# Performance work log

Hardware: AMD Instinct MI355X
Metric: run time of the kernel (lower is better)

The kernel has to match this reference:

```python
import jax, jax.numpy as jnp
import numpy as np

N_NODES = 50000
N_EDGES = 800000
D_IN = 1024
D_OUT = 256
LEAKY_SLOPE = 0.01  # F.leaky_relu default


def setup_inputs() -> dict:
    key = jax.random.key(0)
    k_x, k_w, k_b, k_src, k_dst, k_ew, k_norm = jax.random.split(key, 7)
    x = jax.random.normal(k_x, (N_NODES, D_IN), dtype=jnp.float32)
    # xavier_uniform-style scale for the weight
    limit = np.sqrt(6.0 / (D_IN + D_OUT)).astype(np.float32)
    weight = jax.random.uniform(k_w, (D_IN, D_OUT), dtype=jnp.float32, minval=-limit, maxval=limit)
    stdv = 1.0 / np.sqrt(D_OUT)
    bias = jax.random.uniform(k_b, (D_OUT,), dtype=jnp.float32, minval=-stdv, maxval=stdv)
    src = jax.random.randint(k_src, (N_EDGES,), 0, N_NODES, dtype=jnp.int64)
    dst = jax.random.randint(k_dst, (N_EDGES,), 0, N_NODES, dtype=jnp.int64)
    edge_index = jnp.stack([src, dst], axis=0)  # [2, E]
    edge_weight = jax.random.uniform(k_ew, (N_EDGES,), dtype=jnp.float32)
    norm = jax.random.uniform(k_norm, (N_NODES, 1), dtype=jnp.float32) + 0.5  # avoid div-by-~0
    return {"x": x, "weight": weight, "bias": bias, "edge_index": edge_index,
            "edge_weight": edge_weight, "norm": norm}


def reference(x, weight, bias, edge_index, edge_weight, norm):
    # support = input @ W            [N, D_OUT]
    support = x @ weight
    src = edge_index[0]
    dst = edge_index[1]
    # spmm(adj, support): out[i] = sum_{e: dst_e == i} w_e * support[src_e]
    msgs = support[src] * edge_weight[:, None]            # [E, D_OUT]
    out = jax.ops.segment_sum(msgs, dst, num_segments=x.shape[0])  # [N, D_OUT]
    out = out / norm + bias
    return jax.nn.leaky_relu(out, negative_slope=LEAKY_SLOPE)
```

## Files before the change

kernel.cpp:

```cpp
#include <hip/hip_runtime.h>
#include <hip/hip_bf16.h>

#define N_NODES 50000
#define N_EDGES 800000
#define D_IN    1024
#define D_OUT   256
#define CAP     64
#define LEAKY   0.01f

typedef __attribute__((ext_vector_type(8))) short bf16x8;
typedef __attribute__((ext_vector_type(4))) float f32x4;
typedef __attribute__((ext_vector_type(4))) int   i32x4;
typedef unsigned short u16;

__device__ __forceinline__ u16 f2bfu(float f) {
  uint32_t x = __float_as_uint(f);
  uint32_t r = (x + 0x7FFFu + ((x >> 16) & 1u)) >> 16;
  return (u16)r;
}
__device__ __forceinline__ float bfu2f(u16 u) {
  return __uint_as_float(((uint32_t)u) << 16);
}
__device__ __forceinline__ int swz(int b) { return b ^ (((b >> 7) & 7) << 4); }

__device__ __forceinline__ void gll16(const void* g, void* l) {
  __builtin_amdgcn_global_load_lds(
      (const __attribute__((address_space(1))) uint32_t*)g,
      (__attribute__((address_space(3))) uint32_t*)l, 16, 0, 0);
}

__global__ __launch_bounds__(256) void wconv_kernel(const float* __restrict__ w,
                                                    char* __restrict__ img,
                                                    int* __restrict__ deg) {
  const int t   = blockIdx.x * 256 + threadIdx.x;
  if (t < N_NODES) deg[t] = 0;
  const int t2 = t + 32768;
  if (t2 < N_NODES) deg[t2] = 0;

  const int n   = t & 255;
  const int kc  = (t >> 8) * 8;
  const int kt  = kc >> 6;
  const int kin = kc & 63;
  bf16x8 v;
#pragma unroll
  for (int i = 0; i < 8; ++i) v[i] = (short)f2bfu(w[(size_t)(kc + i) * D_OUT + n]);
  *(bf16x8*)(img + kt * 32768 + swz(n * 128 + kin * 2)) = v;
}

#define BM 64
#define BK 64
#define KSTEPS (D_IN / BK)
#define GEMM_BLOCKS ((N_NODES + BM - 1) / BM)
#define BUILD_BLOCKS 64

__global__ __launch_bounds__(512) void gemm_build_kernel(
    const float* __restrict__ x, const char* __restrict__ img,
    u16* __restrict__ support,
    const int* __restrict__ ei, const float* __restrict__ ew,
    int* __restrict__ deg, int2* __restrict__ csr) {
  __shared__ u16 Wbuf[2][16384];
  __shared__ u16 Xbuf[2][4096];

  if (blockIdx.x < BUILD_BLOCKS) {
    const int t0 = blockIdx.x * 512 + threadIdx.x;
    for (int e = t0; e < N_EDGES; e += BUILD_BLOCKS * 512) {
      const int src = ei[e];
      const int dst = ei[N_EDGES + e];
      const float w = ew[e];
      const int slot = atomicAdd(&deg[dst], 1);
      if (slot < CAP) {
        csr[dst * CAP + slot] = make_int2(src, __float_as_int(w));
      }
    }
    return;
  }

  const int tid  = threadIdx.x;
  const int lane = tid & 63;
  const int wid  = tid >> 6;
  const int wn   = wid & 3;
  const int wm   = wid >> 2;
  const int l15  = lane & 15;
  const int l16  = lane >> 4;
  const int m0   = (blockIdx.x - BUILD_BLOCKS) * BM;

  f32x4 acc[4][2];
#pragma unroll
  for (int i = 0; i < 4; ++i)
#pragma unroll
    for (int j = 0; j < 2; ++j) acc[i][j] = (f32x4)0.0f;

  const int xrow = tid >> 3;
  const int xk8  = (tid & 7) * 8;
  const int xrg  = min(m0 + xrow, N_NODES - 1);
  const float* xp = x + (size_t)xrg * D_IN + xk8;
  const int xw_off = swz(xrow * 128 + xk8 * 2);

  int a_off[2][4], b_off[2][2];
#pragma unroll
  for (int ks = 0; ks < 2; ++ks) {
#pragma unroll
    for (int i = 0; i < 4; ++i)
      a_off[ks][i] = swz((wn * 64 + i * 16 + l15) * 128 + ks * 64 + l16 * 16);
#pragma unroll
    for (int j = 0; j < 2; ++j)
      b_off[ks][j] = swz((wm * 32 + j * 16 + l15) * 128 + ks * 64 + l16 * 16);
  }

#pragma unroll
  for (int r = 0; r < 4; ++r)
    gll16(img + r * 8192 + tid * 16, (char*)&Wbuf[0][0] + r * 8192 + tid * 16);
  {
    const float4 xa = *(const float4*)(xp);
    const float4 xb = *(const float4*)(xp + 4);
    bf16x8 xv;
    xv[0] = (short)f2bfu(xa.x); xv[1] = (short)f2bfu(xa.y);
    xv[2] = (short)f2bfu(xa.z); xv[3] = (short)f2bfu(xa.w);
    xv[4] = (short)f2bfu(xb.x); xv[5] = (short)f2bfu(xb.y);
    xv[6] = (short)f2bfu(xb.z); xv[7] = (short)f2bfu(xb.w);
    *(bf16x8*)((char*)&Xbuf[0][0] + xw_off) = xv;
  }
  __syncthreads();

  for (int kt = 0; kt < KSTEPS; ++kt) {
    const int cur = kt & 1;
    float4 xa, xb;
    if (kt < KSTEPS - 1) {
#pragma unroll
      for (int r = 0; r < 4; ++r)
        gll16(img + (size_t)(kt + 1) * 32768 + r * 8192 + tid * 16,
              (char*)&Wbuf[cur ^ 1][0] + r * 8192 + tid * 16);
      xa = *(const float4*)(xp + (kt + 1) * BK);
      xb = *(const float4*)(xp + (kt + 1) * BK + 4);
    }

#pragma unroll
    for (int ks = 0; ks < 2; ++ks) {
      bf16x8 af[4], bfr[2];
#pragma unroll
      for (int i = 0; i < 4; ++i)
        af[i] = *(const bf16x8*)((const char*)&Wbuf[cur][0] + a_off[ks][i]);
#pragma unroll
      for (int j = 0; j < 2; ++j)
        bfr[j] = *(const bf16x8*)((const char*)&Xbuf[cur][0] + b_off[ks][j]);
#pragma unroll
      for (int i = 0; i < 4; ++i)
#pragma unroll
        for (int j = 0; j < 2; ++j)
          acc[i][j] = __builtin_amdgcn_mfma_f32_16x16x32_bf16(af[i], bfr[j], acc[i][j], 0, 0, 0);
    }

    if (kt < KSTEPS - 1) {
      bf16x8 xv;
      xv[0] = (short)f2bfu(xa.x); xv[1] = (short)f2bfu(xa.y);
      xv[2] = (short)f2bfu(xa.z); xv[3] = (short)f2bfu(xa.w);
      xv[4] = (short)f2bfu(xb.x); xv[5] = (short)f2bfu(xb.y);
      xv[6] = (short)f2bfu(xb.z); xv[7] = (short)f2bfu(xb.w);
      *(bf16x8*)((char*)&Xbuf[cur ^ 1][0] + xw_off) = xv;
    }
    __syncthreads();
  }

#pragma unroll
  for (int j = 0; j < 2; ++j) {
    const int m = m0 + wm * 32 + j * 16 + l15;
    if (m < N_NODES) {
#pragma unroll
      for (int i = 0; i < 4; ++i) {
        const int n = wn * 64 + i * 16 + l16 * 4;
        ushort4 o;
        o.x = f2bfu(acc[i][j][0]);
        o.y = f2bfu(acc[i][j][1]);
        o.z = f2bfu(acc[i][j][2]);
        o.w = f2bfu(acc[i][j][3]);
        *(ushort4*)&support[(size_t)m * D_OUT + n] = o;
      }
    }
  }
}

__global__ __launch_bounds__(256) void agg_kernel(const u16* __restrict__ support,
                                                  const int* __restrict__ deg,
                                                  const int2* __restrict__ csr,
                                                  const float* __restrict__ norm,
                                                  const float* __restrict__ bias,
                                                  float* __restrict__ out) {
  const int lane = threadIdx.x & 63;
  const int wid  = threadIdx.x >> 6;
  const int node = blockIdx.x * 4 + wid;
  const int d    = min(deg[node], CAP);
  const int cb   = node * CAP;
  const int ch   = lane * 4;

  float a0 = 0.f, a1 = 0.f, a2 = 0.f, a3 = 0.f;
  int s = 0;

  for (; s + 16 <= d; s += 16) {
    i32x4 q[8];
#pragma unroll
    for (int i = 0; i < 8; ++i)
      q[i] = __builtin_nontemporal_load((const i32x4*)&csr[cb + s + 2 * i]);
    ushort4 v[16];
#pragma unroll
    for (int i = 0; i < 8; ++i) {
      v[2 * i]     = *(const ushort4*)&support[(size_t)q[i][0] * D_OUT + ch];
      v[2 * i + 1] = *(const ushort4*)&support[(size_t)q[i][2] * D_OUT + ch];
    }
#pragma unroll
    for (int i = 0; i < 8; ++i) {
      const float wa = __int_as_float(q[i][1]);
      const float wb = __int_as_float(q[i][3]);
      a0 = fmaf(wa, bfu2f(v[2 * i].x), a0);
      a1 = fmaf(wa, bfu2f(v[2 * i].y), a1);
      a2 = fmaf(wa, bfu2f(v[2 * i].z), a2);
      a3 = fmaf(wa, bfu2f(v[2 * i].w), a3);
      a0 = fmaf(wb, bfu2f(v[2 * i + 1].x), a0);
      a1 = fmaf(wb, bfu2f(v[2 * i + 1].y), a1);
      a2 = fmaf(wb, bfu2f(v[2 * i + 1].z), a2);
      a3 = fmaf(wb, bfu2f(v[2 * i + 1].w), a3);
    }
  }

  for (; s + 8 <= d; s += 8) {
    i32x4 q[4];
#pragma unroll
    for (int i = 0; i < 4; ++i)
      q[i] = __builtin_nontemporal_load((const i32x4*)&csr[cb + s + 2 * i]);
    ushort4 v[8];
#pragma unroll
    for (int i = 0; i < 4; ++i) {
      v[2 * i]     = *(const ushort4*)&support[(size_t)q[i][0] * D_OUT + ch];
      v[2 * i + 1] = *(const ushort4*)&support[(size_t)q[i][2] * D_OUT + ch];
    }
#pragma unroll
    for (int i = 0; i < 4; ++i) {
      const float wa = __int_as_float(q[i][1]);
      const float wb = __int_as_float(q[i][3]);
      a0 = fmaf(wa, bfu2f(v[2 * i].x), a0);
      a1 = fmaf(wa, bfu2f(v[2 * i].y), a1);
      a2 = fmaf(wa, bfu2f(v[2 * i].z), a2);
      a3 = fmaf(wa, bfu2f(v[2 * i].w), a3);
      a0 = fmaf(wb, bfu2f(v[2 * i + 1].x), a0);
      a1 = fmaf(wb, bfu2f(v[2 * i + 1].y), a1);
      a2 = fmaf(wb, bfu2f(v[2 * i + 1].z), a2);
      a3 = fmaf(wb, bfu2f(v[2 * i + 1].w), a3);
    }
  }

  for (; s < d; ++s) {
    const int2  e   = csr[cb + s];
    const float wgt = __int_as_float(e.y);
    const ushort4 v = *(const ushort4*)&support[(size_t)e.x * D_OUT + ch];
    a0 = fmaf(wgt, bfu2f(v.x), a0);
    a1 = fmaf(wgt, bfu2f(v.y), a1);
    a2 = fmaf(wgt, bfu2f(v.z), a2);
    a3 = fmaf(wgt, bfu2f(v.w), a3);
  }

  const float rn = 1.0f / norm[node];
  const float4 b = *(const float4*)&bias[ch];
  float o0 = fmaf(a0, rn, b.x);
  float o1 = fmaf(a1, rn, b.y);
  float o2 = fmaf(a2, rn, b.z);
  float o3 = fmaf(a3, rn, b.w);
  o0 = o0 > 0.f ? o0 : o0 * LEAKY;
  o1 = o1 > 0.f ? o1 : o1 * LEAKY;
  o2 = o2 > 0.f ? o2 : o2 * LEAKY;
  o3 = o3 > 0.f ? o3 : o3 * LEAKY;
  f32x4 ov;
  ov[0] = o0; ov[1] = o1; ov[2] = o2; ov[3] = o3;
  __builtin_nontemporal_store(ov, (f32x4*)&out[(size_t)node * D_OUT + ch]);
}

extern "C" void kernel_launch(void* const* d_in, const int* in_sizes, int n_in,
                              void* d_out, int out_size, void* d_ws, size_t ws_size,
                              hipStream_t stream) {
  const float* x    = (const float*)d_in[0];
  const float* w    = (const float*)d_in[1];
  const float* bias = (const float*)d_in[2];
  const int*   ei   = (const int*)d_in[3];
  const float* ew   = (const float*)d_in[4];
  const float* norm = (const float*)d_in[5];
  float* out = (float*)d_out;

  char* ws = (char*)d_ws;
  u16*   support = (u16*)  (ws);
  char*  img     =         (ws + 25600000);
  int2*  csr     = (int2*) (ws + 26124288);
  int*   deg     = (int*)  (ws + 51724288);

  wconv_kernel<<<128, 256, 0, stream>>>(w, img, deg);
  gemm_build_kernel<<<BUILD_BLOCKS + GEMM_BLOCKS, 512, 0, stream>>>(
      x, img, support, ei, ew, deg, csr);
  agg_kernel<<<N_NODES / 4, 256, 0, stream>>>(support, deg, csr, norm, bias, out);
}
```

Baseline: 150.1 us.

## Stage full X tile in LDS once and stream fragment-ordered W from global

The weight image is repacked into MFMA fragment order so each wave reads its A fragments straight from global/L2 with coalesced 16-byte loads, dropping the W LDS double buffer. The whole 64x1024 X tile is converted to bf16 and written into LDS up front with nontemporal loads, which removes the per-k-step barriers. The main loop is software-pipelined with register double buffering. In exchange it uses 128KB of LDS per block, which limits occupancy to one block per CU, and each wave reissues W loads from L2 without LDS sharing across the wm waves.

```diff
diff --git a/kernel.cpp b/kernel.cpp
--- a/kernel.cpp
+++ b/kernel.cpp
@@ -21,35 +21,31 @@
 __device__ __forceinline__ float bfu2f(u16 u) {
   return __uint_as_float(((uint32_t)u) << 16);
 }
-__device__ __forceinline__ int swz(int b) { return b ^ (((b >> 7) & 7) << 4); }
-
-__device__ __forceinline__ void gll16(const void* g, void* l) {
-  __builtin_amdgcn_global_load_lds(
-      (const __attribute__((address_space(1))) uint32_t*)g,
-      (__attribute__((address_space(3))) uint32_t*)l, 16, 0, 0);
-}
+__device__ __forceinline__ int swz2(int b) { return b ^ (((b >> 11) & 7) << 4); }
 
 __global__ __launch_bounds__(256) void wconv_kernel(const float* __restrict__ w,
                                                     char* __restrict__ img,
                                                     int* __restrict__ deg) {
-  const int t   = blockIdx.x * 256 + threadIdx.x;
+  const int t = blockIdx.x * 256 + threadIdx.x;
   if (t < N_NODES) deg[t] = 0;
-  const int t2 = t + 32768;
-  if (t2 < N_NODES) deg[t2] = 0;
-
-  const int n   = t & 255;
-  const int kc  = (t >> 8) * 8;
-  const int kt  = kc >> 6;
-  const int kin = kc & 63;
+  const int t2z = t + 32768;
+  if (t2z < N_NODES) deg[t2z] = 0;
+
+  const int s   = t >> 13;
+  const int r13 = t & 8191;
+  const int tt  = r13 >> 8;
+  const int rem = r13 & 255;
+  const int i   = rem >> 6;
+  const int ln  = rem & 63;
+  const int n   = s * 64 + i * 16 + (ln & 15);
+  const int k0  = tt * 32 + (ln >> 4) * 8;
   bf16x8 v;
 #pragma unroll
-  for (int i = 0; i < 8; ++i) v[i] = (short)f2bfu(w[(size_t)(kc + i) * D_OUT + n]);
-  *(bf16x8*)(img + kt * 32768 + swz(n * 128 + kin * 2)) = v;
+  for (int j = 0; j < 8; ++j) v[j] = (short)f2bfu(w[(size_t)(k0 + j) * D_OUT + n]);
+  *(bf16x8*)(img + (size_t)t * 16) = v;
 }
 
 #define BM 64
-#define BK 64
-#define KSTEPS (D_IN / BK)
 #define GEMM_BLOCKS ((N_NODES + BM - 1) / BM)
 #define BUILD_BLOCKS 64
 
@@ -58,8 +54,7 @@
     u16* __restrict__ support,
     const int* __restrict__ ei, const float* __restrict__ ew,
     int* __restrict__ deg, int2* __restrict__ csr) {
-  __shared__ u16 Wbuf[2][16384];
-  __shared__ u16 Xbuf[2][4096];
+  __shared__ char Xlds[BM * 2048];
 
   if (blockIdx.x < BUILD_BLOCKS) {
     const int t0 = blockIdx.x * 512 + threadIdx.x;
@@ -68,9 +63,7 @@
       const int dst = ei[N_EDGES + e];
       const float w = ew[e];
       const int slot = atomicAdd(&deg[dst], 1);
-      if (slot < CAP) {
-        csr[dst * CAP + slot] = make_int2(src, __float_as_int(w));
-      }
+      if (slot < CAP) csr[dst * CAP + slot] = make_int2(src, __float_as_int(w));
     }
     return;
   }
@@ -84,81 +77,68 @@
   const int l16  = lane >> 4;
   const int m0   = (blockIdx.x - BUILD_BLOCKS) * BM;
 
+  {
+    const int row  = tid >> 3;
+    const int col8 = (tid & 7) * 8;
+    const int xr   = min(m0 + row, N_NODES - 1);
+    const float* xp = x + (size_t)xr * D_IN + col8;
+#pragma unroll
+    for (int c = 0; c < 16; ++c) {
+      const f32x4 a = __builtin_nontemporal_load((const f32x4*)(xp + c * 64));
+      const f32x4 b = __builtin_nontemporal_load((const f32x4*)(xp + c * 64 + 4));
+      bf16x8 v;
+      v[0] = (short)f2bfu(a[0]); v[1] = (short)f2bfu(a[1]);
+      v[2] = (short)f2bfu(a[2]); v[3] = (short)f2bfu(a[3]);
+      v[4] = (short)f2bfu(b[0]); v[5] = (short)f2bfu(b[1]);
+      v[6] = (short)f2bfu(b[2]); v[7] = (short)f2bfu(b[3]);
+      *(bf16x8*)(Xlds + swz2(row * 2048 + c * 128 + col8 * 2)) = v;
+    }
+  }
+  __syncthreads();
+
   f32x4 acc[4][2];
 #pragma unroll
   for (int i = 0; i < 4; ++i)
 #pragma unroll
     for (int j = 0; j < 2; ++j) acc[i][j] = (f32x4)0.0f;
 
-  const int xrow = tid >> 3;
-  const int xk8  = (tid & 7) * 8;
-  const int xrg  = min(m0 + xrow, N_NODES - 1);
-  const float* xp = x + (size_t)xrg * D_IN + xk8;
-  const int xw_off = swz(xrow * 128 + xk8 * 2);
-
-  int a_off[2][4], b_off[2][2];
-#pragma unroll
-  for (int ks = 0; ks < 2; ++ks) {
-#pragma unroll
-    for (int i = 0; i < 4; ++i)
-      a_off[ks][i] = swz((wn * 64 + i * 16 + l15) * 128 + ks * 64 + l16 * 16);
+  const char* wp = img + (size_t)wn * 131072 + lane * 16;
+  int xoff[2];
+#pragma unroll
+  for (int j = 0; j < 2; ++j)
+    xoff[j] = (wm * 32 + j * 16 + l15) * 2048 + l16 * 16;
+
+  bf16x8 afA[4], afB[4], bbA[2], bbB[2];
+#pragma unroll
+  for (int i = 0; i < 4; ++i) afA[i] = *(const bf16x8*)(wp + i * 1024);
+#pragma unroll
+  for (int j = 0; j < 2; ++j) bbA[j] = *(const bf16x8*)(Xlds + swz2(xoff[j]));
+
+  for (int t = 0; t < 32; t += 2) {
+#pragma unroll
+    for (int i = 0; i < 4; ++i)
+      afB[i] = *(const bf16x8*)(wp + (t + 1) * 4096 + i * 1024);
 #pragma unroll
     for (int j = 0; j < 2; ++j)
-      b_off[ks][j] = swz((wm * 32 + j * 16 + l15) * 128 + ks * 64 + l16 * 16);
-  }
-
-#pragma unroll
-  for (int r = 0; r < 4; ++r)
-    gll16(img + r * 8192 + tid * 16, (char*)&Wbuf[0][0] + r * 8192 + tid * 16);
-  {
-    const float4 xa = *(const float4*)(xp);
-    const float4 xb = *(const float4*)(xp + 4);
-    bf16x8 xv;
-    xv[0] = (short)f2bfu(xa.x); xv[1] = (short)f2bfu(xa.y);
-    xv[2] = (short)f2bfu(xa.z); xv[3] = (short)f2bfu(xa.w);
-    xv[4] = (short)f2bfu(xb.x); xv[5] = (short)f2bfu(xb.y);
-    xv[6] = (short)f2bfu(xb.z); xv[7] = (short)f2bfu(xb.w);
-    *(bf16x8*)((char*)&Xbuf[0][0] + xw_off) = xv;
-  }
-  __syncthreads();
-
-  for (int kt = 0; kt < KSTEPS; ++kt) {
-    const int cur = kt & 1;
-    float4 xa, xb;
-    if (kt < KSTEPS - 1) {
-#pragma unroll
-      for (int r = 0; r < 4; ++r)
-        gll16(img + (size_t)(kt + 1) * 32768 + r * 8192 + tid * 16,
-              (char*)&Wbuf[cur ^ 1][0] + r * 8192 + tid * 16);
-      xa = *(const float4*)(xp + (kt + 1) * BK);
-      xb = *(const float4*)(xp + (kt + 1) * BK + 4);
-    }
-
-#pragma unroll
-    for (int ks = 0; ks < 2; ++ks) {
-      bf16x8 af[4], bfr[2];
+      bbB[j] = *(const bf16x8*)(Xlds + swz2(xoff[j] + (t + 1) * 64));
+#pragma unroll
+    for (int i = 0; i < 4; ++i)
+#pragma unroll
+      for (int j = 0; j < 2; ++j)
+        acc[i][j] = __builtin_amdgcn_mfma_f32_16x16x32_bf16(afA[i], bbA[j], acc[i][j], 0, 0, 0);
+    if (t < 30) {
 #pragma unroll
       for (int i = 0; i < 4; ++i)
-        af[i] = *(const bf16x8*)((const char*)&Wbuf[cur][0] + a_off[ks][i]);
+        afA[i] = *(const bf16x8*)(wp + (t + 2) * 4096 + i * 1024);
 #pragma unroll
       for (int j = 0; j < 2; ++j)
-        bfr[j] = *(const bf16x8*)((const char*)&Xbuf[cur][0] + b_off[ks][j]);
-#pragma unroll
-      for (int i = 0; i < 4; ++i)
-#pragma unroll
-        for (int j = 0; j < 2; ++j)
-          acc[i][j] = __builtin_amdgcn_mfma_f32_16x16x32_bf16(af[i], bfr[j], acc[i][j], 0, 0, 0);
-    }
-
-    if (kt < KSTEPS - 1) {
-      bf16x8 xv;
-      xv[0] = (short)f2bfu(xa.x); xv[1] = (short)f2bfu(xa.y);
-      xv[2] = (short)f2bfu(xa.z); xv[3] = (short)f2bfu(xa.w);
-      xv[4] = (short)f2bfu(xb.x); xv[5] = (short)f2bfu(xb.y);
-      xv[6] = (short)f2bfu(xb.z); xv[7] = (short)f2bfu(xb.w);
-      *(bf16x8*)((char*)&Xbuf[cur ^ 1][0] + xw_off) = xv;
-    }
-    __syncthreads();
+        bbA[j] = *(const bf16x8*)(Xlds + swz2(xoff[j] + (t + 2) * 64));
+    }
+#pragma unroll
+    for (int i = 0; i < 4; ++i)
+#pragma unroll
+      for (int j = 0; j < 2; ++j)
+        acc[i][j] = __builtin_amdgcn_mfma_f32_16x16x32_bf16(afB[i], bbB[j], acc[i][j], 0, 0, 0);
   }
 
 #pragma unroll
```

After: 183.0 us. 22.0% more time.

## Triple-buffer GEMM K-loop with counted vmcnt waits

Applied to the files above, without the earlier changes.

Moves the GEMM K-loop from double to triple buffering in LDS for both the weight and x tiles. Global loads are issued two tiles ahead, and the barrier uses a counted vmcnt wait instead of a full drain, so loads overlap more of the MFMA work. The cost is extra LDS per block (about 1.5x), which can lower occupancy. The hand-written waitcnt and the clamped redundant loads at the tail also add correctness risk.

```diff
diff --git a/kernel.cpp b/kernel.cpp
--- a/kernel.cpp
+++ b/kernel.cpp
@@ -58,8 +58,8 @@
     u16* __restrict__ support,
     const int* __restrict__ ei, const float* __restrict__ ew,
     int* __restrict__ deg, int2* __restrict__ csr) {
-  __shared__ u16 Wbuf[2][16384];
-  __shared__ u16 Xbuf[2][4096];
+  __shared__ u16 Wbuf[3][16384];
+  __shared__ u16 Xbuf[3][4096];
 
   if (blockIdx.x < BUILD_BLOCKS) {
     const int t0 = blockIdx.x * 512 + threadIdx.x;
@@ -68,9 +68,7 @@
       const int dst = ei[N_EDGES + e];
       const float w = ew[e];
       const int slot = atomicAdd(&deg[dst], 1);
-      if (slot < CAP) {
-        csr[dst * CAP + slot] = make_int2(src, __float_as_int(w));
-      }
+      if (slot < CAP) csr[dst * CAP + slot] = make_int2(src, __float_as_int(w));
     }
     return;
   }
@@ -107,59 +105,85 @@
       b_off[ks][j] = swz((wm * 32 + j * 16 + l15) * 128 + ks * 64 + l16 * 16);
   }
 
-#pragma unroll
-  for (int r = 0; r < 4; ++r)
-    gll16(img + r * 8192 + tid * 16, (char*)&Wbuf[0][0] + r * 8192 + tid * 16);
-  {
-    const float4 xa = *(const float4*)(xp);
-    const float4 xb = *(const float4*)(xp + 4);
-    bf16x8 xv;
-    xv[0] = (short)f2bfu(xa.x); xv[1] = (short)f2bfu(xa.y);
-    xv[2] = (short)f2bfu(xa.z); xv[3] = (short)f2bfu(xa.w);
-    xv[4] = (short)f2bfu(xb.x); xv[5] = (short)f2bfu(xb.y);
-    xv[6] = (short)f2bfu(xb.z); xv[7] = (short)f2bfu(xb.w);
-    *(bf16x8*)((char*)&Xbuf[0][0] + xw_off) = xv;
-  }
-  __syncthreads();
-
-  for (int kt = 0; kt < KSTEPS; ++kt) {
-    const int cur = kt & 1;
-    float4 xa, xb;
-    if (kt < KSTEPS - 1) {
-#pragma unroll
-      for (int r = 0; r < 4; ++r)
-        gll16(img + (size_t)(kt + 1) * 32768 + r * 8192 + tid * 16,
-              (char*)&Wbuf[cur ^ 1][0] + r * 8192 + tid * 16);
-      xa = *(const float4*)(xp + (kt + 1) * BK);
-      xb = *(const float4*)(xp + (kt + 1) * BK + 4);
-    }
-
-#pragma unroll
-    for (int ks = 0; ks < 2; ++ks) {
-      bf16x8 af[4], bfr[2];
-#pragma unroll
-      for (int i = 0; i < 4; ++i)
-        af[i] = *(const bf16x8*)((const char*)&Wbuf[cur][0] + a_off[ks][i]);
-#pragma unroll
-      for (int j = 0; j < 2; ++j)
-        bfr[j] = *(const bf16x8*)((const char*)&Xbuf[cur][0] + b_off[ks][j]);
-#pragma unroll
-      for (int i = 0; i < 4; ++i)
-#pragma unroll
-        for (int j = 0; j < 2; ++j)
-          acc[i][j] = __builtin_amdgcn_mfma_f32_16x16x32_bf16(af[i], bfr[j], acc[i][j], 0, 0, 0);
-    }
-
-    if (kt < KSTEPS - 1) {
-      bf16x8 xv;
-      xv[0] = (short)f2bfu(xa.x); xv[1] = (short)f2bfu(xa.y);
-      xv[2] = (short)f2bfu(xa.z); xv[3] = (short)f2bfu(xa.w);
-      xv[4] = (short)f2bfu(xb.x); xv[5] = (short)f2bfu(xb.y);
-      xv[6] = (short)f2bfu(xb.z); xv[7] = (short)f2bfu(xb.w);
-      *(bf16x8*)((char*)&Xbuf[cur ^ 1][0] + xw_off) = xv;
-    }
-    __syncthreads();
-  }
+  float4 xr[3][2];
+
+#define XLOAD(set, tile) do {                                              \
+    const int kcl_ = min((tile), KSTEPS - 1);                              \
+    xr[set][0] = *(const float4*)(xp + kcl_ * BK);                         \
+    xr[set][1] = *(const float4*)(xp + kcl_ * BK + 4);                     \
+  } while (0)
+
+#define WSTAGE(buf, tile) do {                                             \
+    const int kcl_ = min((tile), KSTEPS - 1);                              \
+    _Pragma("unroll")                                                      \
+    for (int r_ = 0; r_ < 4; ++r_)                                         \
+      gll16(img + kcl_ * 32768 + r_ * 8192 + tid * 16,                     \
+            (char*)&Wbuf[buf][0] + r_ * 8192 + tid * 16);                  \
+  } while (0)
+
+#define XCVT(set, buf) do {                                                \
+    bf16x8 xv_;                                                            \
+    xv_[0] = (short)f2bfu(xr[set][0].x); xv_[1] = (short)f2bfu(xr[set][0].y); \
+    xv_[2] = (short)f2bfu(xr[set][0].z); xv_[3] = (short)f2bfu(xr[set][0].w); \
+    xv_[4] = (short)f2bfu(xr[set][1].x); xv_[5] = (short)f2bfu(xr[set][1].y); \
+    xv_[6] = (short)f2bfu(xr[set][1].z); xv_[7] = (short)f2bfu(xr[set][1].w); \
+    *(bf16x8*)((char*)&Xbuf[buf][0] + xw_off) = xv_;                       \
+  } while (0)
+
+#define MFMA_TILE(buf) do {                                                \
+    _Pragma("unroll")                                                      \
+    for (int ks_ = 0; ks_ < 2; ++ks_) {                                    \
+      bf16x8 af_[4], bf_[2];                                               \
+      _Pragma("unroll")                                                    \
+      for (int i_ = 0; i_ < 4; ++i_)                                       \
+        af_[i_] = *(const bf16x8*)((const char*)&Wbuf[buf][0] + a_off[ks_][i_]); \
+      _Pragma("unroll")                                                    \
+      for (int j_ = 0; j_ < 2; ++j_)                                       \
+        bf_[j_] = *(const bf16x8*)((const char*)&Xbuf[buf][0] + b_off[ks_][j_]); \
+      _Pragma("unroll")                                                    \
+      for (int i_ = 0; i_ < 4; ++i_)                                       \
+        _Pragma("unroll")                                                  \
+        for (int j_ = 0; j_ < 2; ++j_)                                     \
+          acc[i_][j_] = __builtin_amdgcn_mfma_f32_16x16x32_bf16(           \
+              af_[i_], bf_[j_], acc[i_][j_], 0, 0, 0);                     \
+    }                                                                      \
+  } while (0)
+
+#define SYNC_COUNTED() do {                                                \
+    asm volatile("s_waitcnt vmcnt(6)" ::: "memory");                       \
+    __builtin_amdgcn_sched_barrier(0);                                     \
+    asm volatile("s_waitcnt lgkmcnt(0)" ::: "memory");                     \
+    __builtin_amdgcn_s_barrier();                                          \
+  } while (0)
+
+#define BODY(bc, kt) do {                                                  \
+    XLOAD((bc + 2) % 3, (kt) + 2);                                         \
+    WSTAGE((bc + 2) % 3, (kt) + 2);                                        \
+    MFMA_TILE(bc);                                                         \
+    XCVT((bc + 1) % 3, (bc + 1) % 3);                                      \
+    SYNC_COUNTED();                                                        \
+  } while (0)
+
+  XLOAD(0, 0);
+  WSTAGE(0, 0);
+  XLOAD(1, 1);
+  WSTAGE(1, 1);
+  XCVT(0, 0);
+  SYNC_COUNTED();
+
+  for (int kt = 0; kt < KSTEPS - 1; kt += 3) {
+    BODY(0, kt);
+    BODY(1, kt + 1);
+    BODY(2, kt + 2);
+  }
+  MFMA_TILE(0);
+
+#undef XLOAD
+#undef WSTAGE
+#undef XCVT
+#undef MFMA_TILE
+#undef SYNC_COUNTED
+#undef BODY
 
 #pragma unroll
   for (int j = 0; j < 2; ++j) {
```

Measured after the change: 168.4 us. 1.12x slower.
